# Kernel tuning notes

Hardware: AMD Instinct MI355X
Metric: run time of the kernel (lower is better)

Reference implementation:

```python
import jax, jax.numpy as jnp
import numpy as np

B, T, N, D = 2, 10, 1024, 1024
NH = 16
HD = D // NH


def setup_inputs() -> dict:
    key = jax.random.key(0)
    ks = jax.random.split(key, 9)
    data = jax.random.normal(ks[0], (B, N, D), jnp.float32)
    traj_pos = jax.random.normal(ks[1], (B, T, N, 3), jnp.float32)
    q = jax.random.normal(ks[2], (B, T, N, 4), jnp.float32)
    traj_quat = q / (jnp.linalg.norm(q, axis=-1, keepdims=True) + 1e-10)
    certainty = jax.random.uniform(ks[3], (B, N), jnp.float32)
    s = 1.0 / np.sqrt(D).astype(np.float32)
    Wq = jax.random.normal(ks[4], (D, D), jnp.float32) * s
    Wk = jax.random.normal(ks[5], (D, D), jnp.float32) * s
    Wv = jax.random.normal(ks[6], (D, D), jnp.float32) * s
    Wo = jax.random.normal(ks[7], (D, D), jnp.float32) * s
    z = jnp.zeros((D,), jnp.float32)
    return {"data": data, "traj_pos": traj_pos, "traj_quat": traj_quat,
            "certainty": certainty, "Wq": Wq, "bq": z, "Wk": Wk, "bk": z,
            "Wv": Wv, "bv": z, "Wo": Wo, "bo": z}


def reference(data, traj_pos, traj_quat, certainty, Wq, bq, Wk, bk, Wv, bv, Wo, bo):
    b, n, d = data.shape
    # --- trajectory similarity scores (same for all batches: torch.mean over batch+time) ---
    # pos_dist[i,j] = mean_{b,t} ||p_bti - p_btj||
    pd = jnp.linalg.norm(traj_pos[:, :, :, None, :] - traj_pos[:, :, None, :, :], axis=-1).mean(axis=(0, 1))  # (n,n)
    qdm = jnp.linalg.norm(traj_quat[:, :, :, None, :] - traj_quat[:, :, None, :, :], axis=-1).mean(axis=(0, 1))
    qdp = jnp.linalg.norm(traj_quat[:, :, :, None, :] + traj_quat[:, :, None, :, :], axis=-1).mean(axis=(0, 1))
    qd = jnp.minimum(qdm, qdp)
    traj = jnp.exp(-pd - qd)
    traj = traj / traj.sum(axis=-1, keepdims=True)  # (n,n) row-normalized

    def proj(x, W, bias):
        return (x @ W.T + bias).reshape(b, n, NH, HD).transpose(0, 2, 1, 3)  # (b,h,n,hd)

    Q = proj(data, Wq, bq)
    K = proj(data, Wk, bk)
    V = proj(data, Wv, bv)
    scores = jnp.einsum('bhid,bhjd->bhij', Q, K) / np.sqrt(HD).astype(np.float32)
    combined = scores + 0.5 * traj[None, None]  # broadcast over (batch, heads)
    attn = jax.nn.softmax(combined, axis=-1)
    out = jnp.einsum('bhij,bhjd->bhid', attn, V).transpose(0, 2, 1, 3).reshape(b, n, d)
    out = out @ Wo.T + bo
    # certainty update from attention entropy
    avg_attn = attn.mean(axis=1)  # (b,n,n)
    p = jnp.clip(avg_attn, 1e-10, None)
    Hent = -jnp.sum(p * jnp.log(p), axis=-1)  # (b,n)
    H_max = np.log(n).astype(np.float32)
    new_certainty = jnp.maximum(certainty, jax.nn.sigmoid(H_max - Hent))
    return out, new_certainty
```

## Files before the change

### kernel.cpp

```cpp
#include <hip/hip_runtime.h>
#include <math.h>

#define NB 2
#define NN 1024
#define DD 1024
#define NHH 16
#define HDD 64
#define BTT 20

typedef unsigned short u16;
typedef short bf16x8 __attribute__((ext_vector_type(8)));
typedef float f32x4 __attribute__((ext_vector_type(4)));

#define HMAXL 6.93147180559945f
#define C1 0.18033688011112042f
#define TLC 0.72134752044448170f
#define KC  0.072134752044448170f
#define CH 520

#define TRAJ_OFF 0
#define TL_OFF    1048576
#define DATAB_OFF 1572864
#define WQB_OFF   2621440
#define WKB_OFF   3145728
#define WVB_OFF   3670016
#define WOB_OFF   4194304
#define QB_OFF    4718592
#define KB_OFF    5767168
#define VT_OFF    6815744
#define AOB_OFF   7864320
#define LV_OFF    8912896
#define HPART_OFF 8945664
#define RSP_OFF   8978432

__device__ __forceinline__ float b2f(u16 h) { return __uint_as_float(((unsigned)h) << 16); }
__device__ __forceinline__ u16 f2bf(float f) {
  unsigned u = __float_as_uint(f);
  return (u16)((u + 0x7fffu + ((u >> 16) & 1u)) >> 16);
}
__device__ __forceinline__ void dma16(const void* g, void* l) {
  __builtin_amdgcn_global_load_lds((const __attribute__((address_space(1))) void*)g,
                                   (__attribute__((address_space(3))) void*)l, 16, 0, 0);
}

__global__ __launch_bounds__(256) void conv_kernel(const float* __restrict__ data,
                                                   const float* __restrict__ w0,
                                                   const float* __restrict__ w1,
                                                   const float* __restrict__ w2,
                                                   const float* __restrict__ w3,
                                                   u16* __restrict__ dd,
                                                   u16* __restrict__ d0, u16* __restrict__ d1,
                                                   u16* __restrict__ d2, u16* __restrict__ d3) {
  int z = blockIdx.y;
  const float* s;
  u16* d;
  size_t off = 0;
  if (z < 2) { s = data; d = dd; off = (size_t)z * 1048576; }
  else if (z == 2) { s = w0; d = d0; }
  else if (z == 3) { s = w1; d = d1; }
  else if (z == 4) { s = w2; d = d2; }
  else { s = w3; d = d3; }
  size_t i = off + (size_t)(blockIdx.x * 256 + threadIdx.x) * 4;
  float4 v = *(const float4*)(s + i);
  ushort4 o = {f2bf(v.x), f2bf(v.y), f2bf(v.z), f2bf(v.w)};
  *(ushort4*)(d + i) = o;
}

__global__ __launch_bounds__(256) void trajA_kernel(const float* __restrict__ pos,
                                                    const float* __restrict__ quat,
                                                    float* __restrict__ w,
                                                    float* __restrict__ rsp) {
  const int tid = threadIdx.x;
  const int jx = blockIdx.x;
  const int j = jx * 256 + tid;
  const int i0 = blockIdx.y * 8;
  __shared__ float ld[8][BTT][8];
  __shared__ float wredS[4][8];
  if (tid < 8 * BTT) {
    int ii = tid / BTT, bt = tid % BTT;
    const float* pp = pos + ((size_t)bt * NN + i0 + ii) * 3;
    ld[ii][bt][0] = pp[0]; ld[ii][bt][1] = pp[1]; ld[ii][bt][2] = pp[2];
    *(float4*)&ld[ii][bt][4] = *(const float4*)(quat + ((size_t)bt * NN + i0 + ii) * 4);
  }
  __syncthreads();
  float acc[8] = {};
  for (int bt = 0; bt < BTT; ++bt) {
    const float* pj = pos + ((size_t)bt * NN + j) * 3;
    float pjx = pj[0], pjy = pj[1], pjz = pj[2];
    float4 qj = *(const float4*)(quat + ((size_t)bt * NN + j) * 4);
#pragma unroll
    for (int ii = 0; ii < 8; ++ii) {
      float4 pi = *(const float4*)&ld[ii][bt][0];
      float4 qi = *(const float4*)&ld[ii][bt][4];
      float dx = pi.x - pjx, dy = pi.y - pjy, dz = pi.z - pjz;
      float d2 = fmaf(dz, dz, fmaf(dy, dy, dx * dx));
      float dot = fmaf(qi.w, qj.w, fmaf(qi.z, qj.z, fmaf(qi.y, qj.y, qi.x * qj.x)));
      float tq = fmaf(-2.f, fabsf(dot), 2.f);
      acc[ii] += sqrtf(d2) + sqrtf(fmaxf(tq, 0.f));
    }
  }
  const int wv = tid >> 6;
#pragma unroll
  for (int ii = 0; ii < 8; ++ii) {
    float v = exp2f(-acc[ii] * KC);
    w[(size_t)(i0 + ii) * NN + j] = v;
    float s = v;
#pragma unroll
    for (int off = 1; off < 64; off <<= 1) s += __shfl_xor(s, off, 64);
    if ((tid & 63) == 0) wredS[wv][ii] = s;
  }
  __syncthreads();
  if (tid < 8)
    rsp[jx * 1024 + i0 + tid] = wredS[0][tid] + wredS[1][tid] + wredS[2][tid] + wredS[3][tid];
}

__global__ __launch_bounds__(256) void qkv_trajB_kernel(const u16* __restrict__ Ab,
                                                        const u16* __restrict__ Wq,
                                                        const u16* __restrict__ Wk,
                                                        const u16* __restrict__ Wv,
                                                        const float* __restrict__ bq,
                                                        const float* __restrict__ bk,
                                                        const float* __restrict__ bv,
                                                        u16* __restrict__ Qb,
                                                        u16* __restrict__ Kb,
                                                        u16* __restrict__ VtT,
                                                        const float* __restrict__ wtr,
                                                        const float* __restrict__ rsp,
                                                        u16* __restrict__ tl) {
  const int tid = threadIdx.x;
  __shared__ __align__(16) u16 As[128 * 32];
  __shared__ __align__(16) u16 Bs[128 * 32];
  if (blockIdx.x >= 384) {
    int base = (blockIdx.x - 384) * 4;
#pragma unroll
    for (int r = 0; r < 4; ++r) {
      int i = base + r;
      float inv = TLC / (rsp[i] + rsp[1024 + i] + rsp[2048 + i] + rsp[3072 + i]);
      float4 w4 = *(const float4*)(wtr + (size_t)i * NN + tid * 4);
      ushort4 o = {f2bf(w4.x * inv), f2bf(w4.y * inv), f2bf(w4.z * inv), f2bf(w4.w * inv)};
      *(ushort4*)(tl + (size_t)i * NN + tid * 4) = o;
    }
    return;
  }
  const int z = blockIdx.x >> 7;
  const int rem = blockIdx.x & 127;
  const int bxg = rem & 7, byg = rem >> 3;
  const u16* Wb = z == 0 ? Wq : (z == 1 ? Wk : Wv);
  const float* bias = z == 0 ? bq : (z == 1 ? bk : bv);
  const int w = tid >> 6, l = tid & 63, g = l >> 4, ln = l & 15;
  const int bm = byg << 7, bn = bxg << 7;
  const int srow = w * 16 + (l >> 2);
  const int scol = (l & 3) * 8;
  const u16* Ap0 = Ab + (size_t)(bm + srow) * DD + scol;
  const u16* Ap1 = Ab + (size_t)(bm + 64 + srow) * DD + scol;
  const u16* Bp0 = Wb + (size_t)(bn + srow) * DD + scol;
  const u16* Bp1 = Wb + (size_t)(bn + 64 + srow) * DD + scol;
  u16* dA0 = As + w * 512;
  u16* dA1 = As + 2048 + w * 512;
  u16* dB0 = Bs + w * 512;
  u16* dB1 = Bs + 2048 + w * 512;
  const int mw = (w & 1) * 64, nw = (w >> 1) * 64;
  f32x4 zero4 = {0.f, 0.f, 0.f, 0.f};
  f32x4 acc[4][4];
#pragma unroll
  for (int mt = 0; mt < 4; ++mt)
#pragma unroll
    for (int nt = 0; nt < 4; ++nt) acc[mt][nt] = zero4;
  for (int k0 = 0; k0 < DD; k0 += 32) {
    __syncthreads();
    dma16(Ap0 + k0, dA0); dma16(Ap1 + k0, dA1);
    dma16(Bp0 + k0, dB0); dma16(Bp1 + k0, dB1);
    __syncthreads();
    bf16x8 bfr[4], afr[4];
#pragma unroll
    for (int nt = 0; nt < 4; ++nt)
      bfr[nt] = *(const bf16x8*)&Bs[(nw + nt * 16 + ln) * 32 + g * 8];
#pragma unroll
    for (int mt = 0; mt < 4; ++mt)
      afr[mt] = *(const bf16x8*)&As[(mw + mt * 16 + ln) * 32 + g * 8];
#pragma unroll
    for (int mt = 0; mt < 4; ++mt)
#pragma unroll
      for (int nt = 0; nt < 4; ++nt)
        acc[mt][nt] = __builtin_amdgcn_mfma_f32_16x16x32_bf16(afr[mt], bfr[nt], acc[mt][nt], 0, 0, 0);
  }
#pragma unroll
  for (int nt = 0; nt < 4; ++nt) {
    int n = bn + nw + nt * 16 + ln;
    float bb = bias[n];
    if (z == 2) {
      int row = (((bm >> 10) << 4) + (n >> 6)) * 64 + (n & 63);
#pragma unroll
      for (int mt = 0; mt < 4; ++mt) {
        int tok = (bm & 1023) + mw + mt * 16 + g * 4;
        ushort4 pk = {f2bf(acc[mt][nt][0] + bb), f2bf(acc[mt][nt][1] + bb),
                      f2bf(acc[mt][nt][2] + bb), f2bf(acc[mt][nt][3] + bb)};
        *(ushort4*)(VtT + (size_t)row * NN + tok) = pk;
      }
    } else {
      u16* outp = z == 0 ? Qb : Kb;
#pragma unroll
      for (int mt = 0; mt < 4; ++mt) {
#pragma unroll
        for (int r = 0; r < 4; ++r) {
          int m = bm + mw + mt * 16 + g * 4 + r;
          outp[(size_t)m * DD + n] = f2bf(acc[mt][nt][r] + bb);
        }
      }
    }
  }
}

__global__ __launch_bounds__(256) void att_kernel(const u16* __restrict__ Qb,
                                                  const u16* __restrict__ Kb,
                                                  const u16* __restrict__ VtT,
                                                  const u16* __restrict__ tl,
                                                  u16* __restrict__ AOb,
                                                  float* __restrict__ Lv) {
  const int tid = threadIdx.x;
  const int bh = blockIdx.y;
  const int b = bh >> 4, h = bh & 15;
  const int i0 = blockIdx.x << 6;
  const int w = tid >> 6, l = tid & 63, g = l >> 4, ln = l & 15;
  const int wi0 = w * 16;
  __shared__ __align__(16) u16 Qs[8 * CH];
  __shared__ __align__(16) u16 Ks[2][8 * CH];
  __shared__ __align__(16) u16 Vts[2][8 * CH];
  __shared__ __align__(16) u16 Pt[64 * 72];
  __shared__ float lsc[64];
  const int c0 = 2 * w, c1 = 2 * w + 1;
  const int rr = 8 * (l >> 3);
  const int dcol = (l & 7) * 8;
  dma16(Qb + ((size_t)(b * NN) + i0 + c0 + rr) * DD + h * HDD + dcol, Qs + c0 * CH);
  dma16(Qb + ((size_t)(b * NN) + i0 + c1 + rr) * DD + h * HDD + dcol, Qs + c1 * CH);
  const int ig = i0 + wi0 + ln;
  const int lnlo = (ln & 7) * CH;
  const int lnhi = (ln >> 3) * 64;
  f32x4 zero4 = {0.f, 0.f, 0.f, 0.f};
  f32x4 oacc[4];
#pragma unroll
  for (int nt = 0; nt < 4; ++nt) oacc[nt] = zero4;
  float lacc = 0.f;
  for (int j0 = 0; j0 < NN; j0 += 128) {
    __syncthreads();
#pragma unroll
    for (int u = 0; u < 2; ++u) {
      int jb = j0 + u * 64;
      dma16(Kb + ((size_t)(b * NN) + jb + c0 + rr) * DD + h * HDD + dcol, Ks[u] + c0 * CH);
      dma16(Kb + ((size_t)(b * NN) + jb + c1 + rr) * DD + h * HDD + dcol, Ks[u] + c1 * CH);
      dma16(VtT + ((size_t)(bh * 64) + c0 + rr) * NN + jb + dcol, Vts[u] + c0 * CH);
      dma16(VtT + ((size_t)(bh * 64) + c1 + rr) * NN + jb + dcol, Vts[u] + c1 * CH);
    }
    ushort4 tlv[2][4];
#pragma unroll
    for (int u = 0; u < 2; ++u)
#pragma unroll
      for (int jt = 0; jt < 4; ++jt)
        tlv[u][jt] = *(const ushort4*)(tl + (size_t)ig * NN + j0 + u * 64 + jt * 16 + g * 4);
    __syncthreads();
    bf16x8 qf[2];
    qf[0] = *(const bf16x8*)&Qs[lnlo + (2 * w) * 64 + lnhi + g * 8];
    qf[1] = *(const bf16x8*)&Qs[lnlo + (2 * w) * 64 + lnhi + 32 + g * 8];
#pragma unroll
    for (int u = 0; u < 2; ++u) {
      f32x4 sacc[4];
#pragma unroll
      for (int jt = 0; jt < 4; ++jt) {
        sacc[jt] = zero4;
#pragma unroll
        for (int kc = 0; kc < 2; ++kc) {
          bf16x8 af = *(const bf16x8*)&Ks[u][lnlo + (2 * jt) * 64 + lnhi + kc * 32 + g * 8];
          sacc[jt] = __builtin_amdgcn_mfma_f32_16x16x32_bf16(af, qf[kc], sacc[jt], 0, 0, 0);
        }
      }
#pragma unroll
      for (int jt = 0; jt < 4; ++jt) {
        float e0 = exp2f(sacc[jt][0] * C1 + b2f(tlv[u][jt].x));
        float e1 = exp2f(sacc[jt][1] * C1 + b2f(tlv[u][jt].y));
        float e2 = exp2f(sacc[jt][2] * C1 + b2f(tlv[u][jt].z));
        float e3 = exp2f(sacc[jt][3] * C1 + b2f(tlv[u][jt].w));
        lacc += (e0 + e1) + (e2 + e3);
        ushort4 pk = {f2bf(e0), f2bf(e1), f2bf(e2), f2bf(e3)};
        *(ushort4*)(Pt + (wi0 + ln) * 72 + jt * 16 + g * 4) = pk;
      }
      bf16x8 pf[2];
      pf[0] = *(const bf16x8*)&Pt[(wi0 + ln) * 72 + g * 8];
      pf[1] = *(const bf16x8*)&Pt[(wi0 + ln) * 72 + 32 + g * 8];
#pragma unroll
      for (int nt = 0; nt < 4; ++nt) {
#pragma unroll
        for (int kc = 0; kc < 2; ++kc) {
          bf16x8 vf = *(const bf16x8*)&Vts[u][lnlo + (2 * nt) * 64 + lnhi + kc * 32 + g * 8];
          oacc[nt] = __builtin_amdgcn_mfma_f32_16x16x32_bf16(pf[kc], vf, oacc[nt], 0, 0, 0);
        }
      }
    }
  }
  lacc += __shfl_xor(lacc, 16, 64);
  lacc += __shfl_xor(lacc, 32, 64);
  if (g == 0) {
    Lv[(size_t)bh * NN + i0 + wi0 + ln] = lacc;
    lsc[wi0 + ln] = 1.f / lacc;
  }
  __syncthreads();
#pragma unroll
  for (int nt = 0; nt < 4; ++nt) {
    int d = nt * 16 + ln;
#pragma unroll
    for (int r = 0; r < 4; ++r) {
      int i = wi0 + g * 4 + r;
      float v = oacc[nt][r] * lsc[i];
      AOb[((size_t)(b * NN) + i0 + i) * DD + h * HDD + d] = f2bf(v);
    }
  }
}

__global__ __launch_bounds__(256) void ent_o_kernel(const u16* __restrict__ Qb,
                                                    const u16* __restrict__ Kb,
                                                    const u16* __restrict__ tl,
                                                    const float* __restrict__ Lv,
                                                    float* __restrict__ Hp,
                                                    const u16* __restrict__ Ab,
                                                    const u16* __restrict__ Wb,
                                                    const float* __restrict__ bias,
                                                    float* __restrict__ C) {
  const int tid = threadIdx.x;
  __shared__ __align__(16) u16 smem[32 * CH * 2 + 2048];
  const int w = tid >> 6, l = tid & 63, g = l >> 4, ln = l & 15;
  if (blockIdx.x >= 512) {
    const int t = blockIdx.x - 512;
    const int bxg = t & 7, byg = t >> 3;
    u16* As = smem;
    u16* Bs = smem + 4096;
    const int bm = byg << 7, bn = bxg << 7;
    const int srow = w * 16 + (l >> 2);
    const int scol = (l & 3) * 8;
    const u16* Ap0 = Ab + (size_t)(bm + srow) * DD + scol;
    const u16* Ap1 = Ab + (size_t)(bm + 64 + srow) * DD + scol;
    const u16* Bp0 = Wb + (size_t)(bn + srow) * DD + scol;
    const u16* Bp1 = Wb + (size_t)(bn + 64 + srow) * DD + scol;
    u16* dA0 = As + w * 512;
    u16* dA1 = As + 2048 + w * 512;
    u16* dB0 = Bs + w * 512;
    u16* dB1 = Bs + 2048 + w * 512;
    const int mw = (w & 1) * 64, nw = (w >> 1) * 64;
    f32x4 zero4 = {0.f, 0.f, 0.f, 0.f};
    f32x4 acc[4][4];
#pragma unroll
    for (int mt = 0; mt < 4; ++mt)
#pragma unroll
      for (int nt = 0; nt < 4; ++nt) acc[mt][nt] = zero4;
    for (int k0 = 0; k0 < DD; k0 += 32) {
      __syncthreads();
      dma16(Ap0 + k0, dA0); dma16(Ap1 + k0, dA1);
      dma16(Bp0 + k0, dB0); dma16(Bp1 + k0, dB1);
      __syncthreads();
      bf16x8 bfr[4], afr[4];
#pragma unroll
      for (int nt = 0; nt < 4; ++nt)
        bfr[nt] = *(const bf16x8*)&Bs[(nw + nt * 16 + ln) * 32 + g * 8];
#pragma unroll
      for (int mt = 0; mt < 4; ++mt)
        afr[mt] = *(const bf16x8*)&As[(mw + mt * 16 + ln) * 32 + g * 8];
#pragma unroll
      for (int mt = 0; mt < 4; ++mt)
#pragma unroll
        for (int nt = 0; nt < 4; ++nt)
          acc[mt][nt] = __builtin_amdgcn_mfma_f32_16x16x32_bf16(afr[mt], bfr[nt], acc[mt][nt], 0, 0, 0);
    }
#pragma unroll
    for (int nt = 0; nt < 4; ++nt) {
      int n = bn + nw + nt * 16 + ln;
      float bb = bias[n];
#pragma unroll
      for (int mt = 0; mt < 4; ++mt) {
#pragma unroll
        for (int r = 0; r < 4; ++r) {
          int m = bm + mw + mt * 16 + g * 4 + r;
          C[(size_t)m * DD + n] = acc[mt][nt][r] + bb;
        }
      }
    }
    return;
  }
  const int jx = blockIdx.x & 15;
  const int iy = (blockIdx.x >> 4) & 15;
  const int b = blockIdx.x >> 8;
  const int j0 = jx << 6, i0 = iy << 6;
  const int wi0 = w * 16;
  u16* Qs = smem;
  u16* Ks = smem + 32 * CH;
  float* linv = (float*)(smem + 64 * CH);
#pragma unroll
  for (int rep = 0; rep < 4; ++rep) {
    int idx = tid + (rep << 8);
    int hh = idx >> 6, ii = idx & 63;
    linv[hh * 64 + ii] = 1.f / Lv[((size_t)((b << 4) + hh)) * NN + i0 + ii];
  }
  const int rlo = l >> 5;
  const int scol = (l & 31) * 8;
  const int ig = i0 + wi0 + ln;
  const int elo = (ln >> 1) * CH;
  const int ehi = (ln & 1) * 256;
  ushort4 tlv[4];
#pragma unroll
  for (int jt = 0; jt < 4; ++jt)
    tlv[jt] = *(const ushort4*)(tl + (size_t)ig * NN + j0 + jt * 16 + g * 4);
  float P[4][4] = {};
  f32x4 zero4 = {0.f, 0.f, 0.f, 0.f};
  for (int hb = 0; hb < 4; ++hb) {
    __syncthreads();
#pragma unroll
    for (int cc = 0; cc < 8; ++cc) {
      int c = w * 8 + cc;
      dma16(Qb + ((size_t)(b * NN) + i0 + 2 * c + rlo) * DD + hb * 256 + scol, Qs + c * CH);
      dma16(Kb + ((size_t)(b * NN) + j0 + 2 * c + rlo) * DD + hb * 256 + scol, Ks + c * CH);
    }
    __syncthreads();
#pragma unroll
    for (int hl = 0; hl < 4; ++hl) {
      float li = linv[(hb * 4 + hl) * 64 + wi0 + ln];
      bf16x8 qf[2];
      qf[0] = *(const bf16x8*)&Qs[(w * 8) * CH + elo + ehi + hl * 64 + g * 8];
      qf[1] = *(const bf16x8*)&Qs[(w * 8) * CH + elo + ehi + hl * 64 + 32 + g * 8];
#pragma unroll
      for (int jt = 0; jt < 4; ++jt) {
        f32x4 sacc = zero4;
#pragma unroll
        for (int kc = 0; kc < 2; ++kc) {
          bf16x8 af = *(const bf16x8*)&Ks[(jt * 8) * CH + elo + ehi + hl * 64 + kc * 32 + g * 8];
          sacc = __builtin_amdgcn_mfma_f32_16x16x32_bf16(af, qf[kc], sacc, 0, 0, 0);
        }
        P[jt][0] += exp2f(sacc[0] * C1 + b2f(tlv[jt].x)) * li;
        P[jt][1] += exp2f(sacc[1] * C1 + b2f(tlv[jt].y)) * li;
        P[jt][2] += exp2f(sacc[2] * C1 + b2f(tlv[jt].z)) * li;
        P[jt][3] += exp2f(sacc[3] * C1 + b2f(tlv[jt].w)) * li;
      }
    }
  }
  float hs = 0.f;
#pragma unroll
  for (int jt = 0; jt < 4; ++jt) {
#pragma unroll
    for (int r = 0; r < 4; ++r) {
      float p = fmaxf(P[jt][r] * (1.f / NHH), 1e-10f);
      hs -= p * logf(p);
    }
  }
  hs += __shfl_xor(hs, 16, 64);
  hs += __shfl_xor(hs, 32, 64);
  if (g == 0) Hp[jx * 2048 + (size_t)b * NN + i0 + wi0 + ln] = hs;
}

__global__ __launch_bounds__(256) void cert_kernel(const float* __restrict__ Hp,
                                                   const float* __restrict__ cert,
                                                   float* __restrict__ outc) {
  int idx = blockIdx.x * 256 + threadIdx.x;
  float H = 0.f;
#pragma unroll
  for (int jt = 0; jt < 16; ++jt) H += Hp[jt * 2048 + idx];
  float sg = 1.f / (1.f + expf(H - HMAXL));
  outc[idx] = fmaxf(cert[idx], sg);
}

extern "C" void kernel_launch(void* const* d_in, const int* in_sizes, int n_in,
                              void* d_out, int out_size, void* d_ws, size_t ws_size,
                              hipStream_t stream) {
  const float* data      = (const float*)d_in[0];
  const float* traj_pos  = (const float*)d_in[1];
  const float* traj_quat = (const float*)d_in[2];
  const float* certainty = (const float*)d_in[3];
  const float* Wq = (const float*)d_in[4];
  const float* bq = (const float*)d_in[5];
  const float* Wk = (const float*)d_in[6];
  const float* bk = (const float*)d_in[7];
  const float* Wv = (const float*)d_in[8];
  const float* bv = (const float*)d_in[9];
  const float* Wo = (const float*)d_in[10];
  const float* bo = (const float*)d_in[11];

  float* ws = (float*)d_ws;
  float* wtr  = ws + TRAJ_OFF;
  u16* tl    = (u16*)(ws + TL_OFF);
  u16* datab = (u16*)(ws + DATAB_OFF);
  u16* wqb   = (u16*)(ws + WQB_OFF);
  u16* wkb   = (u16*)(ws + WKB_OFF);
  u16* wvb   = (u16*)(ws + WVB_OFF);
  u16* wob   = (u16*)(ws + WOB_OFF);
  u16* Qb    = (u16*)(ws + QB_OFF);
  u16* Kb    = (u16*)(ws + KB_OFF);
  u16* VtT   = (u16*)(ws + VT_OFF);
  u16* AOb   = (u16*)(ws + AOB_OFF);
  float* Lv   = ws + LV_OFF;
  float* Hp   = ws + HPART_OFF;
  float* rsp  = ws + RSP_OFF;
  float* out  = (float*)d_out;
  float* outc = out + (size_t)NB * NN * DD;

  conv_kernel<<<dim3(1024, 6), 256, 0, stream>>>(data, Wq, Wk, Wv, Wo,
                                                 datab, wqb, wkb, wvb, wob);
  trajA_kernel<<<dim3(4, 128), 256, 0, stream>>>(traj_pos, traj_quat, wtr, rsp);
  qkv_trajB_kernel<<<640, 256, 0, stream>>>(datab, wqb, wkb, wvb, bq, bk, bv,
                                            Qb, Kb, VtT, wtr, rsp, tl);
  att_kernel<<<dim3(NN / 64, NB * NHH), 256, 0, stream>>>(Qb, Kb, VtT, tl, AOb, Lv);
  ent_o_kernel<<<640, 256, 0, stream>>>(Qb, Kb, tl, Lv, Hp, AOb, wob, bo, out);
  cert_kernel<<<(NB * NN) / 256, 256, 0, stream>>>(Hp, certainty, outc);
}
```

Baseline: 221.3 us.

## Split entropy and output GEMM kernels, fuse certainty into O-projection launch

Moves the output projection GEMM out of the combined entropy kernel into its own launch, which also carries the certainty update as extra blocks. The entropy kernel now uses static shared memory sized only for its own needs, which may raise occupancy, and the GEMM blocks no longer share a launch with the large-LDS entropy blocks. The trajectory-normalization blocks in the QKV kernel are moved to low block indices so they are scheduled first. This adds no launches overall but serializes entropy and O-projection that previously ran concurrently within one grid.

```diff
diff --git a/kernel.cpp b/kernel.cpp
--- a/kernel.cpp
+++ b/kernel.cpp
@@ -130,8 +130,8 @@
   const int tid = threadIdx.x;
   __shared__ __align__(16) u16 As[128 * 32];
   __shared__ __align__(16) u16 Bs[128 * 32];
-  if (blockIdx.x >= 384) {
-    int base = (blockIdx.x - 384) * 4;
+  if (blockIdx.x < 256) {
+    int base = blockIdx.x * 4;
 #pragma unroll
     for (int r = 0; r < 4; ++r) {
       int i = base + r;
@@ -142,8 +142,9 @@
     }
     return;
   }
-  const int z = blockIdx.x >> 7;
-  const int rem = blockIdx.x & 127;
+  const int bid = blockIdx.x - 256;
+  const int z = bid >> 7;
+  const int rem = bid & 127;
   const int bxg = rem & 7, byg = rem >> 3;
   const u16* Wb = z == 0 ? Wq : (z == 1 ? Wk : Wv);
   const float* bias = z == 0 ? bq : (z == 1 ? bk : bv);
@@ -315,82 +316,21 @@
   }
 }
 
-__global__ __launch_bounds__(256) void ent_o_kernel(const u16* __restrict__ Qb,
-                                                    const u16* __restrict__ Kb,
-                                                    const u16* __restrict__ tl,
-                                                    const float* __restrict__ Lv,
-                                                    float* __restrict__ Hp,
-                                                    const u16* __restrict__ Ab,
-                                                    const u16* __restrict__ Wb,
-                                                    const float* __restrict__ bias,
-                                                    float* __restrict__ C) {
+__global__ __launch_bounds__(256) void ent_kernel(const u16* __restrict__ Qb,
+                                                  const u16* __restrict__ Kb,
+                                                  const u16* __restrict__ tl,
+                                                  const float* __restrict__ Lv,
+                                                  float* __restrict__ Hp) {
   const int tid = threadIdx.x;
-  __shared__ __align__(16) u16 smem[32 * CH * 2 + 2048];
-  const int w = tid >> 6, l = tid & 63, g = l >> 4, ln = l & 15;
-  if (blockIdx.x >= 512) {
-    const int t = blockIdx.x - 512;
-    const int bxg = t & 7, byg = t >> 3;
-    u16* As = smem;
-    u16* Bs = smem + 4096;
-    const int bm = byg << 7, bn = bxg << 7;
-    const int srow = w * 16 + (l >> 2);
-    const int scol = (l & 3) * 8;
-    const u16* Ap0 = Ab + (size_t)(bm + srow) * DD + scol;
-    const u16* Ap1 = Ab + (size_t)(bm + 64 + srow) * DD + scol;
-    const u16* Bp0 = Wb + (size_t)(bn + srow) * DD + scol;
-    const u16* Bp1 = Wb + (size_t)(bn + 64 + srow) * DD + scol;
-    u16* dA0 = As + w * 512;
-    u16* dA1 = As + 2048 + w * 512;
-    u16* dB0 = Bs + w * 512;
-    u16* dB1 = Bs + 2048 + w * 512;
-    const int mw = (w & 1) * 64, nw = (w >> 1) * 64;
-    f32x4 zero4 = {0.f, 0.f, 0.f, 0.f};
-    f32x4 acc[4][4];
-#pragma unroll
-    for (int mt = 0; mt < 4; ++mt)
-#pragma unroll
-      for (int nt = 0; nt < 4; ++nt) acc[mt][nt] = zero4;
-    for (int k0 = 0; k0 < DD; k0 += 32) {
-      __syncthreads();
-      dma16(Ap0 + k0, dA0); dma16(Ap1 + k0, dA1);
-      dma16(Bp0 + k0, dB0); dma16(Bp1 + k0, dB1);
-      __syncthreads();
-      bf16x8 bfr[4], afr[4];
-#pragma unroll
-      for (int nt = 0; nt < 4; ++nt)
-        bfr[nt] = *(const bf16x8*)&Bs[(nw + nt * 16 + ln) * 32 + g * 8];
-#pragma unroll
-      for (int mt = 0; mt < 4; ++mt)
-        afr[mt] = *(const bf16x8*)&As[(mw + mt * 16 + ln) * 32 + g * 8];
-#pragma unroll
-      for (int mt = 0; mt < 4; ++mt)
-#pragma unroll
-        for (int nt = 0; nt < 4; ++nt)
-          acc[mt][nt] = __builtin_amdgcn_mfma_f32_16x16x32_bf16(afr[mt], bfr[nt], acc[mt][nt], 0, 0, 0);
-    }
-#pragma unroll
-    for (int nt = 0; nt < 4; ++nt) {
-      int n = bn + nw + nt * 16 + ln;
-      float bb = bias[n];
-#pragma unroll
-      for (int mt = 0; mt < 4; ++mt) {
-#pragma unroll
-        for (int r = 0; r < 4; ++r) {
-          int m = bm + mw + mt * 16 + g * 4 + r;
-          C[(size_t)m * DD + n] = acc[mt][nt][r] + bb;
-        }
-      }
-    }
-    return;
-  }
   const int jx = blockIdx.x & 15;
   const int iy = (blockIdx.x >> 4) & 15;
   const int b = blockIdx.x >> 8;
   const int j0 = jx << 6, i0 = iy << 6;
+  const int w = tid >> 6, l = tid & 63, g = l >> 4, ln = l & 15;
   const int wi0 = w * 16;
-  u16* Qs = smem;
-  u16* Ks = smem + 32 * CH;
-  float* linv = (float*)(smem + 64 * CH);
+  __shared__ __align__(16) u16 Qs[32 * CH];
+  __shared__ __align__(16) u16 Ks[32 * CH];
+  __shared__ float linv[NHH * 64];
 #pragma unroll
   for (int rep = 0; rep < 4; ++rep) {
     int idx = tid + (rep << 8);
@@ -452,15 +392,76 @@
   if (g == 0) Hp[jx * 2048 + (size_t)b * NN + i0 + wi0 + ln] = hs;
 }
 
-__global__ __launch_bounds__(256) void cert_kernel(const float* __restrict__ Hp,
-                                                   const float* __restrict__ cert,
-                                                   float* __restrict__ outc) {
-  int idx = blockIdx.x * 256 + threadIdx.x;
-  float H = 0.f;
-#pragma unroll
-  for (int jt = 0; jt < 16; ++jt) H += Hp[jt * 2048 + idx];
-  float sg = 1.f / (1.f + expf(H - HMAXL));
-  outc[idx] = fmaxf(cert[idx], sg);
+__global__ __launch_bounds__(256) void gemmo_cert_kernel(const u16* __restrict__ Ab,
+                                                         const u16* __restrict__ Wb,
+                                                         const float* __restrict__ bias,
+                                                         float* __restrict__ C,
+                                                         const float* __restrict__ Hp,
+                                                         const float* __restrict__ cert,
+                                                         float* __restrict__ outc) {
+  const int tid = threadIdx.x;
+  __shared__ __align__(16) u16 As[128 * 32];
+  __shared__ __align__(16) u16 Bs[128 * 32];
+  if (blockIdx.x >= 128) {
+    int idx = (blockIdx.x - 128) * 256 + tid;
+    float H = 0.f;
+#pragma unroll
+    for (int jt = 0; jt < 16; ++jt) H += Hp[jt * 2048 + idx];
+    float sg = 1.f / (1.f + expf(H - HMAXL));
+    outc[idx] = fmaxf(cert[idx], sg);
+    return;
+  }
+  const int bxg = blockIdx.x & 7, byg = blockIdx.x >> 3;
+  const int w = tid >> 6, l = tid & 63, g = l >> 4, ln = l & 15;
+  const int bm = byg << 7, bn = bxg << 7;
+  const int srow = w * 16 + (l >> 2);
+  const int scol = (l & 3) * 8;
+  const u16* Ap0 = Ab + (size_t)(bm + srow) * DD + scol;
+  const u16* Ap1 = Ab + (size_t)(bm + 64 + srow) * DD + scol;
+  const u16* Bp0 = Wb + (size_t)(bn + srow) * DD + scol;
+  const u16* Bp1 = Wb + (size_t)(bn + 64 + srow) * DD + scol;
+  u16* dA0 = As + w * 512;
+  u16* dA1 = As + 2048 + w * 512;
+  u16* dB0 = Bs + w * 512;
+  u16* dB1 = Bs + 2048 + w * 512;
+  const int mw = (w & 1) * 64, nw = (w >> 1) * 64;
+  f32x4 zero4 = {0.f, 0.f, 0.f, 0.f};
+  f32x4 acc[4][4];
+#pragma unroll
+  for (int mt = 0; mt < 4; ++mt)
+#pragma unroll
+    for (int nt = 0; nt < 4; ++nt) acc[mt][nt] = zero4;
+  for (int k0 = 0; k0 < DD; k0 += 32) {
+    __syncthreads();
+    dma16(Ap0 + k0, dA0); dma16(Ap1 + k0, dA1);
+    dma16(Bp0 + k0, dB0); dma16(Bp1 + k0, dB1);
+    __syncthreads();
+    bf16x8 bfr[4], afr[4];
+#pragma unroll
+    for (int nt = 0; nt < 4; ++nt)
+      bfr[nt] = *(const bf16x8*)&Bs[(nw + nt * 16 + ln) * 32 + g * 8];
+#pragma unroll
+    for (int mt = 0; mt < 4; ++mt)
+      afr[mt] = *(const bf16x8*)&As[(mw + mt * 16 + ln) * 32 + g * 8];
+#pragma unroll
+    for (int mt = 0; mt < 4; ++mt)
+#pragma unroll
+      for (int nt = 0; nt < 4; ++nt)
+        acc[mt][nt] = __builtin_amdgcn_mfma_f32_16x16x32_bf16(afr[mt], bfr[nt], acc[mt][nt], 0, 0, 0);
+  }
+#pragma unroll
+  for (int nt = 0; nt < 4; ++nt) {
+    int n = bn + nw + nt * 16 + ln;
+    float bb = bias[n];
+#pragma unroll
+    for (int mt = 0; mt < 4; ++mt) {
+#pragma unroll
+      for (int r = 0; r < 4; ++r) {
+        int m = bm + mw + mt * 16 + g * 4 + r;
+        C[(size_t)m * DD + n] = acc[mt][nt][r] + bb;
+      }
+    }
+  }
 }
 
 extern "C" void kernel_launch(void* const* d_in, const int* in_sizes, int n_in,
@@ -503,6 +504,6 @@
   qkv_trajB_kernel<<<640, 256, 0, stream>>>(datab, wqb, wkb, wvb, bq, bk, bv,
                                             Qb, Kb, VtT, wtr, rsp, tl);
   att_kernel<<<dim3(NN / 64, NB * NHH), 256, 0, stream>>>(Qb, Kb, VtT, tl, AOb, Lv);
-  ent_o_kernel<<<640, 256, 0, stream>>>(Qb, Kb, tl, Lv, Hp, AOb, wob, bo, out);
-  cert_kernel<<<(NB * NN) / 256, 256, 0, stream>>>(Hp, certainty, outc);
-}
+  ent_kernel<<<512, 256, 0, stream>>>(Qb, Kb, tl, Lv, Hp);
+  gemmo_cert_kernel<<<136, 256, 0, stream>>>(AOb, wob, bo, out, Hp, certainty, outc);
+}
```

Result: no change. 221.1 us (-0.1%).
